# Kernel tuning notes

Measured on AMD Instinct MI355X. Metric: run time of the kernel, lower is better.

The kernel has to match this reference:

```python
import jax, jax.numpy as jnp
import numpy as np

N, E, D, H, C = 50000, 1600000, 128, 2, 32

def setup_inputs() -> dict:
    key = jax.random.key(0)
    ks = jax.random.split(key, 8)
    x = jax.random.normal(ks[0], (N, D), jnp.float32)
    edge_index = jax.random.randint(ks[1], (2, E), 0, N)
    intra_enrichment_weights = jax.random.uniform(ks[2], (E,), jnp.float32)
    W = jax.random.normal(ks[3], (D, H * C), jnp.float32) * (1.0 / np.sqrt(D))
    att_src = jax.random.normal(ks[4], (H, C), jnp.float32) * 0.1
    att_dst = jax.random.normal(ks[5], (H, C), jnp.float32) * 0.1
    bias = jnp.zeros((H * C,), jnp.float32)
    enrichment_scale = jnp.asarray(0.01, jnp.float32)
    return dict(x=x, edge_index=edge_index,
                intra_enrichment_weights=intra_enrichment_weights,
                W=W, att_src=att_src, att_dst=att_dst, bias=bias,
                enrichment_scale=enrichment_scale)

def reference(x, edge_index, intra_enrichment_weights, W, att_src, att_dst, bias, enrichment_scale):
    n = x.shape[0]
    xf = jax.nn.elu(x)                       # F.elu on input features
    h = (xf @ W).reshape(n, H, C)            # [N, heads, out]
    # GATConv default add_self_loops=True
    loop = jnp.arange(n, dtype=edge_index.dtype)
    src = jnp.concatenate([edge_index[0], loop])
    dst = jnp.concatenate([edge_index[1], loop])
    a_src = jnp.einsum('nhc,hc->nh', h, att_src)   # [N, H]
    a_dst = jnp.einsum('nhc,hc->nh', h, att_dst)
    alpha = jax.nn.leaky_relu(a_src[src] + a_dst[dst], 0.2)  # [E+N, H]
    # softmax over incoming edges per destination node
    m = jax.ops.segment_max(alpha, dst, num_segments=n)
    e = jnp.exp(alpha - m[dst])
    denom = jax.ops.segment_sum(e, dst, num_segments=n)
    p = e / denom[dst]                       # every node has a self-loop -> denom > 0
    out = jax.ops.segment_sum(h[src] * p[:, :, None], dst, num_segments=n)  # [N, H, C]
    out = out.reshape(n, H * C) + bias
    # enrichment bias (scatter-mean of per-edge weights over source nodes)
    s0 = edge_index[0]
    nw = jax.ops.segment_sum(intra_enrichment_weights, s0, num_segments=n)
    cnt = jax.ops.segment_sum(jnp.ones_like(intra_enrichment_weights), s0, num_segments=n)
    nw = nw / jnp.maximum(cnt, 1.0)
    nw = jnp.clip(nw, 0.2, 5.0)
    scale_factor = 0.1 * jax.nn.sigmoid(enrichment_scale)
    return out + scale_factor * (nw[:, None] - 1.0)
```

## Files before the change

### kernel.cpp

```cpp
#include <hip/hip_runtime.h>


typedef unsigned int u32;
typedef unsigned short u16;

#define SLOTS 4864
#define NB_MAX 400

#define XS 136
#define CS 68

typedef __attribute__((ext_vector_type(8))) short short8;
typedef __attribute__((ext_vector_type(4))) float float4v;

__device__ __forceinline__ u16 f2bf(float f) {
    union { float f; u32 u; } v; v.f = f;
    u32 r = v.u + 0x7fffu + ((v.u >> 16) & 1u);
    return (u16)(r >> 16);
}
__device__ __forceinline__ float bf2f(u16 u) {
    union { u32 i; float f; } v; v.i = ((u32)u) << 16; return v.f;
}
__device__ __forceinline__ float bf_lo(u32 u) {
    union { u32 i; float f; } v; v.i = u << 16; return v.f;
}
__device__ __forceinline__ float bf_hi(u32 u) {
    union { u32 i; float f; } v; v.i = u & 0xFFFF0000u; return v.f;
}
__device__ __forceinline__ void bf_split(float v, short& hi, short& lo) {
    u16 h = f2bf(v);
    float hf = bf2f(h);
    hi = (short)h;
    lo = (short)f2bf(v - hf);
}

__global__ void k_init(int* cursA, int* cursB, int nb) {
    int t = threadIdx.x;
    if (t < nb) { cursA[t] = 0; cursB[t] = 0; }
}

__global__ __launch_bounds__(256) void k_node(
    const float* __restrict__ x, const float* __restrict__ Wm,
    const float* __restrict__ att_s, const float* __restrict__ att_d,
    u32* __restrict__ hb32, float* __restrict__ a_src, float* __restrict__ a_dst,
    int nN)
{
    __shared__ __align__(16) short Ah[64 * XS];
    __shared__ __align__(16) short Al[64 * XS];
    __shared__ __align__(16) short Bh[64 * XS];
    __shared__ __align__(16) short Bl[64 * XS];
    float* Cl = (float*)Ah;

    int t = threadIdx.x;
    int n0 = blockIdx.x * 64;

    {
        int f = t & 63, kq = t >> 6;
        for (int kk = 0; kk < 32; ++kk) {
            int k = kq * 32 + kk;
            float wv = Wm[k * 64 + f];
            short hi, lo; bf_split(wv, hi, lo);
            Bh[f * XS + k] = hi; Bl[f * XS + k] = lo;
        }
    }
    for (int j = 0; j < 8; ++j) {
        int idx = t + 256 * j;
        int r = idx >> 5, c4 = idx & 31;
        int gn = n0 + r;
        float4 xv = make_float4(0.f, 0.f, 0.f, 0.f);
        if (gn < nN) xv = ((const float4*)x)[(size_t)gn * 32 + c4];
        float e[4];
        e[0] = xv.x > 0.f ? xv.x : expm1f(xv.x);
        e[1] = xv.y > 0.f ? xv.y : expm1f(xv.y);
        e[2] = xv.z > 0.f ? xv.z : expm1f(xv.z);
        e[3] = xv.w > 0.f ? xv.w : expm1f(xv.w);
        short h4[4], l4[4];
#pragma unroll
        for (int i = 0; i < 4; ++i) bf_split(e[i], h4[i], l4[i]);
        *(short4*)&Ah[r * XS + c4 * 4] = make_short4(h4[0], h4[1], h4[2], h4[3]);
        *(short4*)&Al[r * XS + c4 * 4] = make_short4(l4[0], l4[1], l4[2], l4[3]);
    }
    __syncthreads();

    {
        int w = t >> 6, l = t & 63;
        int q = l >> 4, m = l & 15;
        int arow = w * 16 + m;
        float4v acc[4] = {};
#pragma unroll
        for (int ks = 0; ks < 4; ++ks) {
            int k0 = ks * 32 + q * 8;
            short8 ah = *(const short8*)&Ah[arow * XS + k0];
            short8 al = *(const short8*)&Al[arow * XS + k0];
#pragma unroll
            for (int nt = 0; nt < 4; ++nt) {
                short8 bh = *(const short8*)&Bh[(nt * 16 + m) * XS + k0];
                short8 bl = *(const short8*)&Bl[(nt * 16 + m) * XS + k0];
                acc[nt] = __builtin_amdgcn_mfma_f32_16x16x32_bf16(ah, bh, acc[nt], 0, 0, 0);
                acc[nt] = __builtin_amdgcn_mfma_f32_16x16x32_bf16(ah, bl, acc[nt], 0, 0, 0);
                acc[nt] = __builtin_amdgcn_mfma_f32_16x16x32_bf16(al, bh, acc[nt], 0, 0, 0);
            }
        }
        __syncthreads();
#pragma unroll
        for (int nt = 0; nt < 4; ++nt)
#pragma unroll
            for (int r = 0; r < 4; ++r)
                Cl[(w * 16 + q * 4 + r) * CS + nt * 16 + m] = acc[nt][r];
    }
    __syncthreads();

    {
        int nl = t >> 2, fq = t & 3;
        int gn = n0 + nl;
        float ps = 0.f, pd = 0.f;
        if (gn < nN) {
            float hv[16];
#pragma unroll
            for (int i = 0; i < 16; ++i) {
                int f = fq * 16 + i;
                hv[i] = Cl[nl * CS + f];
                ps = fmaf(hv[i], att_s[f], ps);
                pd = fmaf(hv[i], att_d[f], pd);
            }
#pragma unroll
            for (int i = 0; i < 8; ++i) {
                u32 pk = ((u32)f2bf(hv[2 * i + 1]) << 16) | (u32)f2bf(hv[2 * i]);
                hb32[(size_t)gn * 32 + fq * 8 + i] = pk;
            }
        }
        float ps2 = ps + __shfl_xor(ps, 1, 64);
        float pd2 = pd + __shfl_xor(pd, 1, 64);
        if (gn < nN && (fq & 1) == 0) {
            a_src[2 * gn + (fq >> 1)] = ps2;
            a_dst[2 * gn + (fq >> 1)] = pd2;
        }
    }
}

__global__ __launch_bounds__(256) void k_partA(
    const int* __restrict__ ei, const float* __restrict__ wgt,
    int* cursA, int* cursB, u32* bufA, u32* bufB, int E, int nb)
{
    __shared__ int cntA[NB_MAX], basA[NB_MAX], cntB[NB_MAX], basB[NB_MAX];
    int t = threadIdx.x;
    for (int b = t; b < nb; b += 256) { cntA[b] = 0; cntB[b] = 0; }
    __syncthreads();

    int base = blockIdx.x * 4096;
    int sv[16], dv[16]; float wv[16];
#pragma unroll
    for (int k = 0; k < 16; ++k) {
        int e = base + k * 256 + t;
        if (e < E) { sv[k] = ei[e]; dv[k] = ei[E + e]; wv[k] = wgt[e]; }
        else       { sv[k] = -1;    dv[k] = -1;        wv[k] = 0.f; }
    }
#pragma unroll
    for (int k = 0; k < 16; ++k) {
        if (dv[k] >= 0) {
            atomicAdd(&cntA[dv[k] >> 7], 1);
            atomicAdd(&cntB[sv[k] >> 7], 1);
        }
    }
    __syncthreads();
    for (int b = t; b < nb; b += 256) {
        int ca = cntA[b], cb = cntB[b];
        if (ca > 0) basA[b] = atomicAdd(&cursA[b], ca);
        if (cb > 0) basB[b] = atomicAdd(&cursB[b], cb);
        cntA[b] = 0; cntB[b] = 0;
    }
    __syncthreads();
#pragma unroll
    for (int k = 0; k < 16; ++k) {
        if (dv[k] >= 0) {
            int bA = dv[k] >> 7;
            int pA = basA[bA] + atomicAdd(&cntA[bA], 1);
            if (pA < SLOTS)
                bufA[bA * SLOTS + pA] = ((u32)(dv[k] & 127) << 16) | (u32)sv[k];
            int bB = sv[k] >> 7;
            u32 wf = (u32)(wv[k] * 16777216.f);
            if (wf > 0xFFFFFFu) wf = 0xFFFFFFu;
            int pB = basB[bB] + atomicAdd(&cntB[bB], 1);
            if (pB < SLOTS)
                bufB[bB * SLOTS + pB] = ((u32)(sv[k] & 127) << 24) | wf;
        }
    }
}

__global__ __launch_bounds__(256) void k_partB_dst(
    const u32* bufA_in, const int* __restrict__ cursA,
    u32* bufA_out, int* __restrict__ deg, int* __restrict__ offs, int nN)
{
    __shared__ u32 st[SLOTS];
    __shared__ int ldeg[128], lscan[128], lcur[128];
    int b = blockIdx.x, t = threadIdx.x;
    int n = cursA[b]; if (n > SLOTS) n = SLOTS;
    if (t < 128) { ldeg[t] = 0; lcur[t] = 0; }
    __syncthreads();
    for (int i = t; i < n; i += 256) {
        u32 v = bufA_in[b * SLOTS + i];
        st[i] = v;
        atomicAdd(&ldeg[v >> 16], 1);
    }
    __syncthreads();
    if (t < 128) lscan[t] = ldeg[t];
    __syncthreads();
    for (int off = 1; off < 128; off <<= 1) {
        int v = 0;
        if (t < 128 && t >= off) v = lscan[t - off];
        __syncthreads();
        if (t < 128) lscan[t] += v;
        __syncthreads();
    }
    int excl = 0;
    if (t < 128) excl = lscan[t] - ldeg[t];
    __syncthreads();
    if (t < 128) lscan[t] = excl;
    __syncthreads();
    for (int i = t; i < n; i += 256) {
        u32 v = st[i];
        int dl = v >> 16;
        int pos = lscan[dl] + atomicAdd(&lcur[dl], 1);
        bufA_out[b * SLOTS + pos] = v & 0xFFFFu;
    }
    int node = (b << 7) + t;
    if (t < 128 && node < nN) { deg[node] = ldeg[t]; offs[node] = b * SLOTS + lscan[t]; }
}

__global__ __launch_bounds__(256) void k_partB_src(
    const u32* __restrict__ bufB, const int* __restrict__ cursB,
    float* __restrict__ nwv, int nN)
{
    __shared__ u32 usum[128]; __shared__ int ucnt[128];
    int b = blockIdx.x, t = threadIdx.x;
    int n = cursB[b]; if (n > SLOTS) n = SLOTS;
    if (t < 128) { usum[t] = 0; ucnt[t] = 0; }
    __syncthreads();
    for (int i = t; i < n; i += 256) {
        u32 v = bufB[b * SLOTS + i];
        atomicAdd(&usum[v >> 24], v & 0xFFFFFFu);
        atomicAdd(&ucnt[v >> 24], 1);
    }
    __syncthreads();
    int node = (b << 7) + t;
    if (t < 128 && node < nN) {
        float cnt = (float)ucnt[t];
        float nw = ((float)usum[t] * (1.f / 16777216.f)) / fmaxf(cnt, 1.f);
        nwv[node] = fminf(fmaxf(nw, 0.2f), 5.f);
    }
}

__global__ __launch_bounds__(256) void k_accum(
    const u32* __restrict__ hb32,
    const float* __restrict__ a_src, const float* __restrict__ a_dst,
    const u32* __restrict__ esrc, const int* __restrict__ offs,
    const int* __restrict__ deg, const float* __restrict__ nwv,
    const float* __restrict__ bias, const float* __restrict__ esc,
    float* __restrict__ out, int nN)
{
    __shared__ u32 lds[4][2][64][2];
    int tid = threadIdx.x;
    int lane = tid & 63;
    int n = (blockIdx.x * 256 + tid) >> 6;
    if (n >= nN) return;
    int ws = tid >> 6;
    int l31 = lane & 31;
    int half = lane >> 5;
    int head = l31 >> 4;

    float ad0 = a_dst[2 * n], ad1 = a_dst[2 * n + 1];
    float as0 = a_src[2 * n], as1 = a_src[2 * n + 1];
    float t0 = as0 + ad0; t0 = t0 > 0.f ? t0 : 0.2f * t0;
    float t1 = as1 + ad1; t1 = t1 > 0.f ? t1 : 0.2f * t1;
    float es0 = __expf(t0), es1 = __expf(t1);

    u32 hself = hb32[(size_t)n * 32 + l31];
    float eself = head ? es1 : es0;
    float acc0 = half ? 0.f : eself * bf_lo(hself);
    float acc1 = half ? 0.f : eself * bf_hi(hself);
    float dsum0 = 0.f, dsum1 = 0.f;

    int start = offs[n], len = deg[n];
    for (int b0 = 0; b0 < len; b0 += 64) {
        int cnt = min(64, len - b0);
        u32 si = (u32)n; float e0 = 0.f, e1 = 0.f;
        if (lane < cnt) {
            si = esrc[start + b0 + lane];
            float2 ap = ((const float2*)a_src)[si];
            float v0 = ap.x + ad0; v0 = v0 > 0.f ? v0 : 0.2f * v0;
            float v1 = ap.y + ad1; v1 = v1 > 0.f ? v1 : 0.2f * v1;
            e0 = __expf(v0); e1 = __expf(v1);
        }
        dsum0 += e0; dsum1 += e1;
        lds[ws][0][lane][0] = si; lds[ws][0][lane][1] = __float_as_uint(e0);
        lds[ws][1][lane][0] = si; lds[ws][1][lane][1] = __float_as_uint(e1);

        int iters = (cnt + 1) >> 1;
#pragma unroll 4
        for (int k = 0; k < iters; ++k) {
            int e = 2 * k + half;
            u32 rsi = lds[ws][head][e][0];
            float w = __uint_as_float(lds[ws][head][e][1]);
            u32 hv = hb32[(size_t)rsi * 32 + l31];
            acc0 = fmaf(w, bf_lo(hv), acc0);
            acc1 = fmaf(w, bf_hi(hv), acc1);
        }
    }

#pragma unroll
    for (int off = 1; off < 64; off <<= 1) {
        dsum0 += __shfl_xor(dsum0, off, 64);
        dsum1 += __shfl_xor(dsum1, off, 64);
    }
    float den0 = es0 + dsum0, den1 = es1 + dsum1;

    acc0 += __shfl_xor(acc0, 32, 64);
    acc1 += __shfl_xor(acc1, 32, 64);

    if (half == 0) {
        float den = head ? den1 : den0;
        float sf = 0.1f / (1.f + __expf(-esc[0]));
        float en = sf * (nwv[n] - 1.f);
        float2 bb = ((const float2*)bias)[l31];
        float2 o;
        o.x = acc0 / den + bb.x + en;
        o.y = acc1 / den + bb.y + en;
        ((float2*)out)[(size_t)n * 32 + l31] = o;
    }
}

extern "C" void kernel_launch(void* const* d_in, const int* in_sizes, int n_in,
                              void* d_out, int out_size, void* d_ws, size_t ws_size,
                              hipStream_t stream)
{
    const float* x     = (const float*)d_in[0];
    const int*   ei    = (const int*)d_in[1];
    const float* wgt   = (const float*)d_in[2];
    const float* Wm    = (const float*)d_in[3];
    const float* att_s = (const float*)d_in[4];
    const float* att_d = (const float*)d_in[5];
    const float* bias  = (const float*)d_in[6];
    const float* esc   = (const float*)d_in[7];
    float* out = (float*)d_out;

    int nN = in_sizes[0] / 128;
    int E  = in_sizes[2];
    int NB = (nN + 127) / 128;

    char* p = (char*)d_ws;
    auto alloc = [&](size_t bytes) -> char* {
        char* r = p; p += (bytes + 255) & ~(size_t)255; return r;
    };
    u32*   hb32  = (u32*)  alloc((size_t)nN * 32 * 4);
    float* a_src = (float*)alloc((size_t)nN * 2 * 4);
    float* a_dst = (float*)alloc((size_t)nN * 2 * 4);
    int*   deg   = (int*)  alloc((size_t)nN * 4);
    int*   offs  = (int*)  alloc((size_t)nN * 4);
    float* nwv   = (float*)alloc((size_t)nN * 4);
    int*   cursA = (int*)  alloc(NB_MAX * 4);
    int*   cursB = (int*)  alloc(NB_MAX * 4);
    u32*   bufA  = (u32*)  alloc((size_t)NB * SLOTS * 4);
    u32*   bufB  = (u32*)  alloc((size_t)NB * SLOTS * 4);

    int nblkA = (E + 4095) / 4096;

    k_init<<<dim3(1), dim3(512), 0, stream>>>(cursA, cursB, NB);
    k_node<<<dim3((nN + 63) / 64), dim3(256), 0, stream>>>(x, Wm, att_s, att_d, hb32, a_src, a_dst, nN);
    k_partA<<<dim3(nblkA), dim3(256), 0, stream>>>(ei, wgt, cursA, cursB, bufA, bufB, E, NB);
    k_partB_dst<<<dim3(NB), dim3(256), 0, stream>>>(bufA, cursA, bufA, deg, offs, nN);
    k_partB_src<<<dim3(NB), dim3(256), 0, stream>>>(bufB, cursB, nwv, nN);
    k_accum<<<dim3((nN + 3) / 4), dim3(256), 0, stream>>>(hb32, a_src, a_dst, bufA, offs, deg,
                                                          nwv, bias, esc, out, nN);
}
```

Baseline: 199.9 us.

## Stage bucketed edges in LDS to coalesce global scatter writes

k_partA now sorts each block's edges by bucket in shared memory with a local prefix scan over bucket counts, then writes them out in contiguous runs so global stores to bufA/bufB coalesce instead of scattering one element at a time. k_partB_dst likewise builds the per-destination ordering in a second shared buffer and copies it out linearly. The aim is to cut uncoalesced global write traffic. In exchange it adds about 36KB of LDS in partA and a doubled LDS footprint in partB_dst, which may lower occupancy, plus extra barriers for the scans.

```diff
diff --git a/kernel.cpp b/kernel.cpp
--- a/kernel.cpp
+++ b/kernel.cpp
@@ -6,6 +6,7 @@
 
 #define SLOTS 4864
 #define NB_MAX 400
+#define EPB 4096
 
 #define XS 136
 #define CS 68
@@ -142,12 +143,19 @@
     const int* __restrict__ ei, const float* __restrict__ wgt,
     int* cursA, int* cursB, u32* bufA, u32* bufB, int E, int nb)
 {
-    __shared__ int cntA[NB_MAX], basA[NB_MAX], cntB[NB_MAX], basB[NB_MAX];
+    __shared__ u32 arrA[EPB], arrB[EPB];
+    __shared__ u16 bkA[EPB], bkB[EPB];
+    __shared__ int cntA[NB_MAX], cntB[NB_MAX];
+    __shared__ int lofsA[NB_MAX], lofsB[NB_MAX];
+    __shared__ int basA[NB_MAX], basB[NB_MAX];
+    __shared__ int part[256];
+
     int t = threadIdx.x;
     for (int b = t; b < nb; b += 256) { cntA[b] = 0; cntB[b] = 0; }
     __syncthreads();
 
-    int base = blockIdx.x * 4096;
+    int base = blockIdx.x * EPB;
+    int nv = min(EPB, E - base);
     int sv[16], dv[16]; float wv[16];
 #pragma unroll
     for (int k = 0; k < 16; ++k) {
@@ -167,23 +175,66 @@
         int ca = cntA[b], cb = cntB[b];
         if (ca > 0) basA[b] = atomicAdd(&cursA[b], ca);
         if (cb > 0) basB[b] = atomicAdd(&cursB[b], cb);
-        cntA[b] = 0; cntB[b] = 0;
-    }
+    }
+    __syncthreads();
+    {
+        int b0 = 2 * t, b1 = 2 * t + 1;
+        int c0 = (b0 < nb) ? cntA[b0] : 0;
+        int c1 = (b1 < nb) ? cntA[b1] : 0;
+        part[t] = c0 + c1;
+        __syncthreads();
+        for (int off = 1; off < 256; off <<= 1) {
+            int v = (t >= off) ? part[t - off] : 0;
+            __syncthreads();
+            part[t] += v;
+            __syncthreads();
+        }
+        int excl = part[t] - (c0 + c1);
+        if (b0 < nb) lofsA[b0] = excl;
+        if (b1 < nb) lofsA[b1] = excl + c0;
+        __syncthreads();
+        c0 = (b0 < nb) ? cntB[b0] : 0;
+        c1 = (b1 < nb) ? cntB[b1] : 0;
+        part[t] = c0 + c1;
+        __syncthreads();
+        for (int off = 1; off < 256; off <<= 1) {
+            int v = (t >= off) ? part[t - off] : 0;
+            __syncthreads();
+            part[t] += v;
+            __syncthreads();
+        }
+        excl = part[t] - (c0 + c1);
+        if (b0 < nb) lofsB[b0] = excl;
+        if (b1 < nb) lofsB[b1] = excl + c0;
+    }
+    __syncthreads();
+    for (int b = t; b < nb; b += 256) { cntA[b] = 0; cntB[b] = 0; }
     __syncthreads();
 #pragma unroll
     for (int k = 0; k < 16; ++k) {
         if (dv[k] >= 0) {
             int bA = dv[k] >> 7;
-            int pA = basA[bA] + atomicAdd(&cntA[bA], 1);
-            if (pA < SLOTS)
-                bufA[bA * SLOTS + pA] = ((u32)(dv[k] & 127) << 16) | (u32)sv[k];
+            int r = lofsA[bA] + atomicAdd(&cntA[bA], 1);
+            arrA[r] = ((u32)(dv[k] & 127) << 16) | (u32)sv[k];
+            bkA[r] = (u16)bA;
             int bB = sv[k] >> 7;
             u32 wf = (u32)(wv[k] * 16777216.f);
             if (wf > 0xFFFFFFu) wf = 0xFFFFFFu;
-            int pB = basB[bB] + atomicAdd(&cntB[bB], 1);
-            if (pB < SLOTS)
-                bufB[bB * SLOTS + pB] = ((u32)(sv[k] & 127) << 24) | wf;
-        }
+            int r2 = lofsB[bB] + atomicAdd(&cntB[bB], 1);
+            arrB[r2] = ((u32)(sv[k] & 127) << 24) | wf;
+            bkB[r2] = (u16)bB;
+        }
+    }
+    __syncthreads();
+    for (int i = t; i < nv; i += 256) {
+        int bA = bkA[i];
+        int g = basA[bA] + (i - lofsA[bA]);
+        if (g < SLOTS) bufA[bA * SLOTS + g] = arrA[i];
+    }
+    for (int i = t; i < nv; i += 256) {
+        int bB = bkB[i];
+        int g = basB[bB] + (i - lofsB[bB]);
+        if (g < SLOTS) bufB[bB * SLOTS + g] = arrB[i];
     }
 }
 
@@ -192,6 +243,7 @@
     u32* bufA_out, int* __restrict__ deg, int* __restrict__ offs, int nN)
 {
     __shared__ u32 st[SLOTS];
+    __shared__ u32 st2[SLOTS];
     __shared__ int ldeg[128], lscan[128], lcur[128];
     int b = blockIdx.x, t = threadIdx.x;
     int n = cursA[b]; if (n > SLOTS) n = SLOTS;
@@ -221,8 +273,10 @@
         u32 v = st[i];
         int dl = v >> 16;
         int pos = lscan[dl] + atomicAdd(&lcur[dl], 1);
-        bufA_out[b * SLOTS + pos] = v & 0xFFFFu;
-    }
+        st2[pos] = v & 0xFFFFu;
+    }
+    __syncthreads();
+    for (int i = t; i < n; i += 256) bufA_out[b * SLOTS + i] = st2[i];
     int node = (b << 7) + t;
     if (t < 128 && node < nN) { deg[node] = ldeg[t]; offs[node] = b * SLOTS + lscan[t]; }
 }
@@ -362,7 +416,7 @@
     u32*   bufA  = (u32*)  alloc((size_t)NB * SLOTS * 4);
     u32*   bufB  = (u32*)  alloc((size_t)NB * SLOTS * 4);
 
-    int nblkA = (E + 4095) / 4096;
+    int nblkA = (E + EPB - 1) / EPB;
 
     k_init<<<dim3(1), dim3(512), 0, stream>>>(cursA, cursB, NB);
     k_node<<<dim3((nN + 63) / 64), dim3(256), 0, stream>>>(x, Wm, att_s, att_d, hb32, a_src, a_dst, nN);
```

After: 193.9 us. 3.0% less time.
